# Optimization experiments

Measured on AMD Instinct MI355X. Metric: run time of the kernel, lower is better.

The kernel has to match this reference:

```python
import jax, jax.numpy as jnp
import numpy as np

D = 128          # node_state_dim
N_NODES = 5000
WINDOW = 10
N_TOTAL = WINDOW * N_NODES
E = 131072       # structural (int) edges
T = 2            # message passing steps
HID = 1024


def setup_inputs() -> dict:
    key = jax.random.key(0)
    ks = jax.random.split(key, 20)
    ie = jax.random.randint(ks[0], (E, 3), 0, N_NODES, dtype=jnp.int32)
    int_edges = jnp.stack([ie[:, 0] % WINDOW, ie[:, 1], ie[:, 2]], axis=1)
    nodes = jax.random.randint(ks[1], (N_NODES,), 0, 10, dtype=jnp.int32)

    def init(k, shape, scale=0.05):
        return (jax.random.normal(k, shape, jnp.float32) * scale)

    params = dict(
        embed_table=init(ks[2], (10, D)),
        msg_W1=init(ks[3], (2 * D, HID)), msg_b1=jnp.zeros((HID,), jnp.float32),
        msg_W2=init(ks[4], (HID, D)), msg_b2=jnp.zeros((D,), jnp.float32),
        gru_int_W=init(ks[5], (D, 3 * D)), gru_int_U=init(ks[6], (D, 3 * D)),
        gru_int_b=jnp.zeros((2, 3 * D), jnp.float32),
        gru_temp_W=init(ks[7], (D, 3 * D)), gru_temp_U=init(ks[8], (D, 3 * D)),
        gru_temp_b=jnp.zeros((2, 3 * D), jnp.float32),
        ro_W1=init(ks[9], (D, HID)), ro_b1=jnp.zeros((HID,), jnp.float32),
        ro_W2=init(ks[10], (HID, 512)), ro_b2=jnp.zeros((512,), jnp.float32),
        ro_W3=init(ks[11], (512, 10)), ro_b3=jnp.zeros((10,), jnp.float32),
    )
    return {"int_edges": int_edges, "nodes": nodes, **params}


def _temp_edges():
    fwd_src = np.arange(0, N_TOTAL - N_NODES)
    fwd_dst = fwd_src + N_NODES
    bwd_src = np.arange(N_NODES, N_TOTAL)
    bwd_dst = bwd_src - N_NODES
    src = jnp.asarray(np.concatenate([fwd_src, bwd_src]), jnp.int32)
    dst = jnp.asarray(np.concatenate([fwd_dst, bwd_dst]), jnp.int32)
    return src, dst


def _gru(x, h, W, U, b):
    # Keras GRUCell, reset_after=True. x,h: [N,D]; W,U: [D,3D]; b: [2,3D]
    xg = x @ W + b[0]
    hg = h @ U + b[1]
    xz, xr, xh = jnp.split(xg, 3, axis=-1)
    hz, hr, hh = jnp.split(hg, 3, axis=-1)
    z = jax.nn.sigmoid(xz + hz)
    r = jax.nn.sigmoid(xr + hr)
    hcand = jnp.tanh(xh + r * hh)
    return z * h + (1.0 - z) * hcand


def _msg(x, W1, b1, W2, b2):
    # Dense(1024,relu) -> Dropout(inference: identity) -> Dense(D,relu)
    return jax.nn.relu(jax.nn.relu(x @ W1 + b1) @ W2 + b2)


def _seg_mean(x, idx, n):
    s = jax.ops.segment_sum(x, idx, num_segments=n)
    c = jax.ops.segment_sum(jnp.ones((x.shape[0],), x.dtype), idx, num_segments=n)
    return jnp.where(c[:, None] > 0, s / jnp.maximum(c, 1.0)[:, None], 0.0)


def reference(int_edges, nodes, embed_table, msg_W1, msg_b1, msg_W2, msg_b2,
              gru_int_W, gru_int_U, gru_int_b, gru_temp_W, gru_temp_U, gru_temp_b,
              ro_W1, ro_b1, ro_W2, ro_b2, ro_W3, ro_b3):
    node_idx = int_edges[:, 0] * N_NODES + int_edges[:, 1]        # [E]
    neigh_idx = int_edges[:, 0] * N_NODES + int_edges[:, 2]       # [E]
    t_src, t_dst = _temp_edges()

    h = embed_table[nodes]                                        # [n_nodes, D]
    h = jnp.repeat(h, WINDOW, axis=0)                             # [N_TOTAL, D]

    for _ in range(T):
        # structural edges
        m_in = jnp.concatenate([h[node_idx], h[neigh_idx]], axis=1)   # [E, 2D]
        m = _msg(m_in, msg_W1, msg_b1, msg_W2, msg_b2)                # [E, D]
        agg = _seg_mean(m, neigh_idx, N_TOTAL)                        # [N_TOTAL, D]
        h = _gru(agg, h, gru_int_W, gru_int_U, gru_int_b)
        # temporal edges
        tm_in = jnp.concatenate([h[t_src], h[t_dst]], axis=1)
        tm = _msg(tm_in, msg_W1, msg_b1, msg_W2, msg_b2)
        tagg = _seg_mean(tm, t_dst, N_TOTAL)
        h = _gru(tagg, h, gru_temp_W, gru_temp_U, gru_temp_b)

    # readout on first frame's nodes
    x = h[:N_NODES]
    x = jax.nn.relu(x @ ro_W1 + ro_b1)
    x = jax.nn.relu(x @ ro_W2 + ro_b2)
    return jax.nn.softmax(x @ ro_W3 + ro_b3, axis=-1)
```

## Files before the change

kernel.cpp:

```cpp
#include <hip/hip_runtime.h>
#include <math.h>

#define D 128
#define N_NODES 5000
#define WINDOW 10
#define N_TOTAL 50000
#define NE_INT 131072
#define NE_TMP 90000
#define NE_FWD (N_TOTAL - N_NODES)
#define HID 1024

typedef short bf16x8 __attribute__((ext_vector_type(8)));
typedef float f32x4 __attribute__((ext_vector_type(4)));

#define SA 264
#define SH 136
#define SK 136
#define SCAN_B 256

static __device__ __forceinline__ short f2bf(float f) {
    union { float f; unsigned u; } v; v.f = f;
    unsigned r = v.u + 0x7fffu + ((v.u >> 16) & 1u);
    return (short)(r >> 16);
}
static __device__ __forceinline__ float bf2f(short s) {
    union { unsigned u; float f; } v;
    v.u = ((unsigned)(unsigned short)s) << 16;
    return v.f;
}

__global__ void k_tcvt(const float* __restrict__ in, short* __restrict__ out, int K, int N) {
    int i = blockIdx.x * blockDim.x + threadIdx.x;
    if (i >= N * K) return;
    int n = i / K, k = i - n * K;
    out[i] = f2bf(in[(size_t)k * N + n]);
}

__global__ void k_init_h(const int* __restrict__ nodes, const float* __restrict__ embed,
                         float* __restrict__ h32, short* __restrict__ h16) {
    int i = blockIdx.x * blockDim.x + threadIdx.x;
    if (i >= N_TOTAL * D) return;
    int row = i >> 7;
    int c = i & 127;
    int n = nodes[row / WINDOW];
    float v = embed[n * D + c];
    h32[i] = v;
    h16[i] = f2bf(v);
}

__global__ void k_build_int_edges(const int* __restrict__ ie, int* __restrict__ src,
                                  int* __restrict__ dst, int* __restrict__ icnt) {
    int e = blockIdx.x * blockDim.x + threadIdx.x;
    if (e >= NE_INT) return;
    int t = ie[e * 3 + 0], a = ie[e * 3 + 1], b = ie[e * 3 + 2];
    int d = t * N_NODES + b;
    src[e] = t * N_NODES + a;
    dst[e] = d;
    atomicAdd(&icnt[d], 1);
}

__global__ void k_build_tmp_edges(int* __restrict__ src, int* __restrict__ dst) {
    int e = blockIdx.x * blockDim.x + threadIdx.x;
    if (e >= NE_TMP) return;
    int s, d;
    if (e < NE_FWD) { s = e; d = e + N_NODES; }
    else { int q = e - NE_FWD; s = q + N_NODES; d = q; }
    src[e] = s;
    dst[e] = d;
}

__global__ void k_scan_partial(const int* __restrict__ cnt, int* __restrict__ rowstart,
                               int* __restrict__ btot, int n) {
    __shared__ int s[SCAN_B];
    int tid = threadIdx.x;
    int i = blockIdx.x * SCAN_B + tid;
    int v = (i < n) ? cnt[i] : 0;
    s[tid] = v;
    __syncthreads();
    for (int off = 1; off < SCAN_B; off <<= 1) {
        int x = (tid >= off) ? s[tid - off] : 0;
        __syncthreads();
        s[tid] += x;
        __syncthreads();
    }
    if (i < n) rowstart[i] = s[tid] - v;
    if (tid == SCAN_B - 1) btot[blockIdx.x] = s[tid];
}

__global__ void k_scan_block(int* __restrict__ btot, int nb) {
    __shared__ int s[SCAN_B];
    int tid = threadIdx.x;
    int v = (tid < nb) ? btot[tid] : 0;
    s[tid] = v;
    __syncthreads();
    for (int off = 1; off < SCAN_B; off <<= 1) {
        int x = (tid >= off) ? s[tid - off] : 0;
        __syncthreads();
        s[tid] += x;
        __syncthreads();
    }
    if (tid < nb) btot[tid] = s[tid] - v;
}

__global__ void k_scan_add(int* __restrict__ rowstart, const int* __restrict__ btot,
                           int* __restrict__ cursor, int n, int total) {
    int i = blockIdx.x * blockDim.x + threadIdx.x;
    if (i < n) {
        int v = rowstart[i] + btot[i >> 8];
        rowstart[i] = v;
        cursor[i] = v;
    }
    if (i == 0) rowstart[n] = total;
}

__global__ void k_fill_csr(const int* __restrict__ dst, int nE, int* __restrict__ cursor,
                           int* __restrict__ eidx) {
    int e = blockIdx.x * blockDim.x + threadIdx.x;
    if (e >= nE) return;
    int p = atomicAdd(&cursor[dst[e]], 1);
    eidx[p] = e;
}

__global__ void __launch_bounds__(256, 2) k_msg_mfma(
    const short* __restrict__ h16, const int* __restrict__ src, const int* __restrict__ dst,
    int nE, const short* __restrict__ W1T, const float* __restrict__ b1,
    const short* __restrict__ W2T, const float* __restrict__ b2,
    short* __restrict__ m)
{
    __shared__ short Ain[64 * SA];
    __shared__ short Hid[64 * SH];

    int t = threadIdx.x;
    int e0 = blockIdx.x * 64;

    {
        int r = t >> 2, q = t & 3;
        int e = e0 + r;
        int ec = (e < nE) ? e : (nE - 1);
        int s = src[ec], d = dst[ec];
        const uint4* ps = (const uint4*)(h16 + (size_t)s * D);
        const uint4* pd = (const uint4*)(h16 + (size_t)d * D);
        uint4* ao = (uint4*)(Ain + r * SA);
#pragma unroll
        for (int i = 0; i < 8; ++i) {
            int g = i * 4 + q;
            ao[g] = (i < 4) ? ps[g] : pd[g - 16];
        }
    }
    __syncthreads();

    int w = t >> 6, lane = t & 63;
    int lm = lane & 15, lk = lane >> 4;

    f32x4 c2[2][4];
#pragma unroll
    for (int cs = 0; cs < 2; ++cs) {
        int out0 = w * 32 + cs * 16 + lk * 4;
#pragma unroll
        for (int et = 0; et < 4; ++et)
#pragma unroll
            for (int rg = 0; rg < 4; ++rg) c2[cs][et][rg] = b2[out0 + rg];
    }

    for (int hc = 0; hc < 8; ++hc) {
        f32x4 c1[2][4];
#pragma unroll
        for (int cs = 0; cs < 2; ++cs) {
            int ch0 = hc * 128 + (2 * w + cs) * 16 + lk * 4;
#pragma unroll
            for (int et = 0; et < 4; ++et)
#pragma unroll
                for (int rg = 0; rg < 4; ++rg) c1[cs][et][rg] = b1[ch0 + rg];
        }
#pragma unroll
        for (int kk = 0; kk < 8; ++kk) {
            int ko = kk * 32 + lk * 8;
            bf16x8 a0 = *(const bf16x8*)(W1T + (size_t)(hc * 128 + (2 * w) * 16 + lm) * 256 + ko);
            bf16x8 a1 = *(const bf16x8*)(W1T + (size_t)(hc * 128 + (2 * w + 1) * 16 + lm) * 256 + ko);
            bf16x8 bf[4];
#pragma unroll
            for (int et = 0; et < 4; ++et)
                bf[et] = *(const bf16x8*)(Ain + (et * 16 + lm) * SA + ko);
#pragma unroll
            for (int et = 0; et < 4; ++et) {
                c1[0][et] = __builtin_amdgcn_mfma_f32_16x16x32_bf16(a0, bf[et], c1[0][et], 0, 0, 0);
                c1[1][et] = __builtin_amdgcn_mfma_f32_16x16x32_bf16(a1, bf[et], c1[1][et], 0, 0, 0);
            }
        }
        __syncthreads();
#pragma unroll
        for (int cs = 0; cs < 2; ++cs) {
            int ch_in = (2 * w + cs) * 16 + lk * 4;
#pragma unroll
            for (int et = 0; et < 4; ++et) {
                int edge = et * 16 + lm;
                short4 sv;
                sv.x = f2bf(fmaxf(c1[cs][et][0], 0.f));
                sv.y = f2bf(fmaxf(c1[cs][et][1], 0.f));
                sv.z = f2bf(fmaxf(c1[cs][et][2], 0.f));
                sv.w = f2bf(fmaxf(c1[cs][et][3], 0.f));
                *(short4*)(Hid + edge * SH + ch_in) = sv;
            }
        }
        __syncthreads();
#pragma unroll
        for (int kk = 0; kk < 4; ++kk) {
            int ko = kk * 32 + lk * 8;
            bf16x8 a0 = *(const bf16x8*)(W2T + (size_t)(w * 32 + lm) * 1024 + hc * 128 + ko);
            bf16x8 a1 = *(const bf16x8*)(W2T + (size_t)(w * 32 + 16 + lm) * 1024 + hc * 128 + ko);
            bf16x8 bf[4];
#pragma unroll
            for (int et = 0; et < 4; ++et)
                bf[et] = *(const bf16x8*)(Hid + (et * 16 + lm) * SH + ko);
#pragma unroll
            for (int et = 0; et < 4; ++et) {
                c2[0][et] = __builtin_amdgcn_mfma_f32_16x16x32_bf16(a0, bf[et], c2[0][et], 0, 0, 0);
                c2[1][et] = __builtin_amdgcn_mfma_f32_16x16x32_bf16(a1, bf[et], c2[1][et], 0, 0, 0);
            }
        }
    }

#pragma unroll
    for (int et = 0; et < 4; ++et) {
        int edge = et * 16 + lm;
        int e = e0 + edge;
        if (e >= nE) continue;
        short* rowp = m + (size_t)e * 128;
#pragma unroll
        for (int cs = 0; cs < 2; ++cs) {
            int out0 = w * 32 + cs * 16 + lk * 4;
            short4 sv;
            sv.x = f2bf(fmaxf(c2[cs][et][0], 0.f));
            sv.y = f2bf(fmaxf(c2[cs][et][1], 0.f));
            sv.z = f2bf(fmaxf(c2[cs][et][2], 0.f));
            sv.w = f2bf(fmaxf(c2[cs][et][3], 0.f));
            *(short4*)(rowp + out0) = sv;
        }
    }
}

__global__ void __launch_bounds__(256, 2) k_gru_mfma(
    const short* __restrict__ m, const int* __restrict__ rowstart,
    const int* __restrict__ eidx, int mode,
    float* __restrict__ h32, short* __restrict__ h16,
    const short* __restrict__ WT, const short* __restrict__ UT,
    const float* __restrict__ b)
{
    __shared__ short Ax[64 * SK];
    __shared__ short Hx[64 * SK];
    int t = threadIdx.x;
    int r0 = blockIdx.x * 64;

    {
        int r = t >> 2, q = t & 3;
        int row = r0 + r;
        int rc = (row < N_TOTAL) ? row : (N_TOTAL - 1);
        const uint4* hp = (const uint4*)(h16 + (size_t)rc * D);
        uint4* hxo = (uint4*)(Hx + r * SK);
#pragma unroll
        for (int i = 0; i < 4; ++i) hxo[q * 4 + i] = hp[q * 4 + i];

        float acc[32];
#pragma unroll
        for (int i = 0; i < 32; ++i) acc[i] = 0.f;
        int deg = 0;
        if (row < N_TOTAL) {
            if (mode == 0) {
                int s0 = rowstart[row], s1 = rowstart[row + 1];
                deg = s1 - s0;
                for (int p = s0; p < s1; ++p) {
                    int e = eidx[p];
                    const uint4* mp = (const uint4*)(m + (size_t)e * 128 + q * 32);
#pragma unroll
                    for (int i = 0; i < 4; ++i) {
                        uint4 v = mp[i];
                        const short* sp = (const short*)&v;
#pragma unroll
                        for (int j = 0; j < 8; ++j) acc[i * 8 + j] += bf2f(sp[j]);
                    }
                }
            } else {
                if (row >= N_NODES) {
                    const uint4* mp = (const uint4*)(m + (size_t)(row - N_NODES) * 128 + q * 32);
                    ++deg;
#pragma unroll
                    for (int i = 0; i < 4; ++i) {
                        uint4 v = mp[i];
                        const short* sp = (const short*)&v;
#pragma unroll
                        for (int j = 0; j < 8; ++j) acc[i * 8 + j] += bf2f(sp[j]);
                    }
                }
                if (row < NE_FWD) {
                    const uint4* mp = (const uint4*)(m + (size_t)(NE_FWD + row) * 128 + q * 32);
                    ++deg;
#pragma unroll
                    for (int i = 0; i < 4; ++i) {
                        uint4 v = mp[i];
                        const short* sp = (const short*)&v;
#pragma unroll
                        for (int j = 0; j < 8; ++j) acc[i * 8 + j] += bf2f(sp[j]);
                    }
                }
            }
        }
        float inv = (deg > 0) ? 1.f / (float)deg : 0.f;
        uint4* axp = (uint4*)(Ax + r * SK + q * 32);
#pragma unroll
        for (int i = 0; i < 4; ++i) {
            union { uint4 u; short s[8]; } pk;
#pragma unroll
            for (int j = 0; j < 8; ++j) pk.s[j] = f2bf(acc[i * 8 + j] * inv);
            axp[i] = pk.u;
        }
    }
    __syncthreads();

    int w = t >> 6, lane = t & 63;
    int lm = lane & 15, lk = lane >> 4;

    for (int g = 0; g < 8; ++g) {
        int ch = g * 16 + lm;
        f32x4 cxz, cxr, cxh, chz, chr_, chh;
#pragma unroll
        for (int rg = 0; rg < 4; ++rg) {
            cxz[rg] = b[ch];        chz[rg] = b[384 + ch];
            cxr[rg] = b[128 + ch];  chr_[rg] = b[384 + 128 + ch];
            cxh[rg] = b[256 + ch];  chh[rg] = b[384 + 256 + ch];
        }
#pragma unroll
        for (int kk = 0; kk < 4; ++kk) {
            int ko = kk * 32 + lk * 8;
            bf16x8 ax = *(const bf16x8*)(Ax + (w * 16 + lm) * SK + ko);
            bf16x8 hx = *(const bf16x8*)(Hx + (w * 16 + lm) * SK + ko);
            bf16x8 bz = *(const bf16x8*)(WT + (size_t)(ch) * 128 + ko);
            bf16x8 br = *(const bf16x8*)(WT + (size_t)(128 + ch) * 128 + ko);
            bf16x8 bh = *(const bf16x8*)(WT + (size_t)(256 + ch) * 128 + ko);
            bf16x8 uz = *(const bf16x8*)(UT + (size_t)(ch) * 128 + ko);
            bf16x8 ur = *(const bf16x8*)(UT + (size_t)(128 + ch) * 128 + ko);
            bf16x8 uh = *(const bf16x8*)(UT + (size_t)(256 + ch) * 128 + ko);
            cxz = __builtin_amdgcn_mfma_f32_16x16x32_bf16(ax, bz, cxz, 0, 0, 0);
            cxr = __builtin_amdgcn_mfma_f32_16x16x32_bf16(ax, br, cxr, 0, 0, 0);
            cxh = __builtin_amdgcn_mfma_f32_16x16x32_bf16(ax, bh, cxh, 0, 0, 0);
            chz = __builtin_amdgcn_mfma_f32_16x16x32_bf16(hx, uz, chz, 0, 0, 0);
            chr_ = __builtin_amdgcn_mfma_f32_16x16x32_bf16(hx, ur, chr_, 0, 0, 0);
            chh = __builtin_amdgcn_mfma_f32_16x16x32_bf16(hx, uh, chh, 0, 0, 0);
        }
#pragma unroll
        for (int rg = 0; rg < 4; ++rg) {
            int row = r0 + w * 16 + lk * 4 + rg;
            if (row >= N_TOTAL) continue;
            float z = 1.f / (1.f + expf(-(cxz[rg] + chz[rg])));
            float r_ = 1.f / (1.f + expf(-(cxr[rg] + chr_[rg])));
            float hcv = tanhf(cxh[rg] + r_ * chh[rg]);
            size_t idx = (size_t)row * D + ch;
            float hold = h32[idx];
            float hnew = z * hold + (1.f - z) * hcv;
            h32[idx] = hnew;
            h16[idx] = f2bf(hnew);
        }
    }
}

__global__ void __launch_bounds__(256, 2) k_ro_mfma(
    const short* __restrict__ A16, const short* __restrict__ BT,
    const float* __restrict__ bias, float* __restrict__ C32, short* __restrict__ C16,
    int M, int N, int K)
{
    __shared__ short As[64 * SK];
    int t = threadIdx.x;
    int mb = blockIdx.y * 64;
    int nb = blockIdx.x * 128;
    int w = t >> 6, lane = t & 63;
    int lm = lane & 15, lk = lane >> 4;

    f32x4 acc[8];
#pragma unroll
    for (int nt = 0; nt < 8; ++nt) {
        float bv = bias[nb + nt * 16 + lm];
        acc[nt][0] = bv; acc[nt][1] = bv; acc[nt][2] = bv; acc[nt][3] = bv;
    }

    for (int kc = 0; kc < K; kc += 128) {
        __syncthreads();
        {
            int r = t >> 2, q = t & 3;
            int row = mb + r;
            int rc = (row < M) ? row : (M - 1);
            const uint4* ap = (const uint4*)(A16 + (size_t)rc * K + kc);
            uint4* ao = (uint4*)(As + r * SK);
#pragma unroll
            for (int i = 0; i < 4; ++i) ao[i * 4 + q] = ap[i * 4 + q];
        }
        __syncthreads();
#pragma unroll
        for (int kk = 0; kk < 4; ++kk) {
            int ko = kk * 32 + lk * 8;
            bf16x8 a = *(const bf16x8*)(As + (w * 16 + lm) * SK + ko);
#pragma unroll
            for (int nt = 0; nt < 8; ++nt) {
                bf16x8 bfr = *(const bf16x8*)(BT + (size_t)(nb + nt * 16 + lm) * K + kc + ko);
                acc[nt] = __builtin_amdgcn_mfma_f32_16x16x32_bf16(a, bfr, acc[nt], 0, 0, 0);
            }
        }
    }
#pragma unroll
    for (int nt = 0; nt < 8; ++nt) {
        int col = nb + nt * 16 + lm;
#pragma unroll
        for (int rg = 0; rg < 4; ++rg) {
            int row = mb + w * 16 + lk * 4 + rg;
            if (row >= M) continue;
            float v = fmaxf(acc[nt][rg], 0.f);
            if (C32) C32[(size_t)row * N + col] = v;
            if (C16) C16[(size_t)row * N + col] = f2bf(v);
        }
    }
}

__global__ void __launch_bounds__(64) k_logits_softmax(
    const float* __restrict__ r2, const float* __restrict__ W3,
    const float* __restrict__ b3, float* __restrict__ out)
{
    int row = blockIdx.x;
    int t = threadIdx.x;
    float p[10];
#pragma unroll
    for (int j = 0; j < 10; ++j) p[j] = 0.f;
    for (int k = t; k < 512; k += 64) {
        float v = r2[(size_t)row * 512 + k];
#pragma unroll
        for (int j = 0; j < 10; ++j) p[j] += v * W3[k * 10 + j];
    }
#pragma unroll
    for (int j = 0; j < 10; ++j) {
        float s = p[j];
        for (int off = 32; off > 0; off >>= 1) s += __shfl_down(s, off);
        p[j] = s;
    }
    if (t == 0) {
        float mx = -1e30f;
#pragma unroll
        for (int j = 0; j < 10; ++j) { p[j] += b3[j]; mx = fmaxf(mx, p[j]); }
        float sum = 0.f;
#pragma unroll
        for (int j = 0; j < 10; ++j) { p[j] = expf(p[j] - mx); sum += p[j]; }
        float inv = 1.f / sum;
#pragma unroll
        for (int j = 0; j < 10; ++j) out[(size_t)row * 10 + j] = p[j] * inv;
    }
}

extern "C" void kernel_launch(void* const* d_in, const int* in_sizes, int n_in,
                              void* d_out, int out_size, void* d_ws, size_t ws_size,
                              hipStream_t stream)
{
    const int*   ie    = (const int*)d_in[0];
    const int*   nodes = (const int*)d_in[1];
    const float* embed = (const float*)d_in[2];
    const float* mW1   = (const float*)d_in[3];
    const float* mb1   = (const float*)d_in[4];
    const float* mW2   = (const float*)d_in[5];
    const float* mb2   = (const float*)d_in[6];
    const float* giW   = (const float*)d_in[7];
    const float* giU   = (const float*)d_in[8];
    const float* gib   = (const float*)d_in[9];
    const float* gtW   = (const float*)d_in[10];
    const float* gtU   = (const float*)d_in[11];
    const float* gtb   = (const float*)d_in[12];
    const float* rW1   = (const float*)d_in[13];
    const float* rb1   = (const float*)d_in[14];
    const float* rW2   = (const float*)d_in[15];
    const float* rb2   = (const float*)d_in[16];
    const float* rW3   = (const float*)d_in[17];
    const float* rb3   = (const float*)d_in[18];
    float* out = (float*)d_out;

    char* ws = (char*)d_ws;
    size_t off = 0;
    auto alloc = [&](size_t bytes) {
        void* p = ws + off;
        off += (bytes + 255) & ~(size_t)255;
        return p;
    };
    float* h32   = (float*)alloc((size_t)N_TOTAL * D * 4);
    short* h16   = (short*)alloc((size_t)N_TOTAL * D * 2);
    short* m     = (short*)alloc((size_t)NE_INT * 128 * 2);
    int*   icnt  = (int*)alloc((size_t)N_TOTAL * 4);
    int*   rowst = (int*)alloc((size_t)(N_TOTAL + 1) * 4);
    int*   btot  = (int*)alloc(256 * 4);
    int*   curs  = (int*)alloc((size_t)N_TOTAL * 4);
    int*   eidx  = (int*)alloc((size_t)NE_INT * 4);
    int*   srcA  = (int*)alloc((size_t)NE_INT * 4);
    int*   dstA  = (int*)alloc((size_t)NE_INT * 4);
    int*   srcT  = (int*)alloc((size_t)NE_TMP * 4);
    int*   dstT  = (int*)alloc((size_t)NE_TMP * 4);
    short* mW1T  = (short*)alloc((size_t)HID * 256 * 2);
    short* mW2T  = (short*)alloc((size_t)D * HID * 2);
    short* giWT  = (short*)alloc((size_t)384 * D * 2);
    short* giUT  = (short*)alloc((size_t)384 * D * 2);
    short* gtWT  = (short*)alloc((size_t)384 * D * 2);
    short* gtUT  = (short*)alloc((size_t)384 * D * 2);
    short* rW1T  = (short*)alloc((size_t)HID * D * 2);
    short* rW2T  = (short*)alloc((size_t)512 * HID * 2);
    short* r1_16 = (short*)alloc((size_t)N_NODES * HID * 2);
    float* r2_32 = (float*)alloc((size_t)N_NODES * 512 * 4);

    auto tc = [&](const float* in, short* o, int K, int N) {
        k_tcvt<<<(N * K + 255) / 256, 256, 0, stream>>>(in, o, K, N);
    };
    tc(mW1, mW1T, 256, HID);
    tc(mW2, mW2T, HID, D);
    tc(giW, giWT, D, 384);
    tc(giU, giUT, D, 384);
    tc(gtW, gtWT, D, 384);
    tc(gtU, gtUT, D, 384);
    tc(rW1, rW1T, D, HID);
    tc(rW2, rW2T, HID, 512);

    hipMemsetAsync(icnt, 0, (size_t)N_TOTAL * 4, stream);
    k_init_h<<<(N_TOTAL * D + 255) / 256, 256, 0, stream>>>(nodes, embed, h32, h16);
    k_build_int_edges<<<(NE_INT + 255) / 256, 256, 0, stream>>>(ie, srcA, dstA, icnt);
    k_build_tmp_edges<<<(NE_TMP + 255) / 256, 256, 0, stream>>>(srcT, dstT);
    int nb = (N_TOTAL + SCAN_B - 1) / SCAN_B;
    k_scan_partial<<<nb, SCAN_B, 0, stream>>>(icnt, rowst, btot, N_TOTAL);
    k_scan_block<<<1, SCAN_B, 0, stream>>>(btot, nb);
    k_scan_add<<<nb, SCAN_B, 0, stream>>>(rowst, btot, curs, N_TOTAL, NE_INT);
    k_fill_csr<<<(NE_INT + 255) / 256, 256, 0, stream>>>(dstA, NE_INT, curs, eidx);

    int gmsgA = (NE_INT + 63) / 64;
    int gmsgT = (NE_TMP + 63) / 64;
    int ggru = (N_TOTAL + 63) / 64;
    for (int it = 0; it < 2; ++it) {
        k_msg_mfma<<<gmsgA, 256, 0, stream>>>(h16, srcA, dstA, NE_INT, mW1T, mb1, mW2T, mb2, m);
        k_gru_mfma<<<ggru, 256, 0, stream>>>(m, rowst, eidx, 0, h32, h16, giWT, giUT, gib);

        k_msg_mfma<<<gmsgT, 256, 0, stream>>>(h16, srcT, dstT, NE_TMP, mW1T, mb1, mW2T, mb2, m);
        k_gru_mfma<<<ggru, 256, 0, stream>>>(m, rowst, eidx, 1, h32, h16, gtWT, gtUT, gtb);
    }

    dim3 g1(HID / 128, (N_NODES + 63) / 64);
    k_ro_mfma<<<g1, 256, 0, stream>>>(h16, rW1T, rb1, (float*)nullptr, r1_16, N_NODES, HID, D);
    dim3 g2(512 / 128, (N_NODES + 63) / 64);
    k_ro_mfma<<<g2, 256, 0, stream>>>(r1_16, rW2T, rb2, r2_32, (short*)nullptr, N_NODES, 512, HID);
    k_logits_softmax<<<N_NODES, 64, 0, stream>>>(r2_32, rW3, rb3, out);
}
```

Measured before the change: 1.295 ms.

## Keep gathered message inputs in registers and double-buffer swizzled hidden tile

The message MLP kernel now gathers each edge's src/dst node states straight from global memory into MFMA B-fragment registers, so the staging LDS tile and its sync are gone. The hidden-activation LDS tile is double-buffered by chunk parity, which drops one barrier per chunk. It is stored with an XOR swizzle instead of padding to avoid bank conflicts. Biases are added at the ReLU epilogue instead of being used to initialise the accumulators. This holds 32 extra bf16x8 vectors in registers per thread, which raises register pressure under launch_bounds(256,2) and risks spills or lower occupancy.

```diff
diff --git a/kernel.cpp b/kernel.cpp
--- a/kernel.cpp
+++ b/kernel.cpp
@@ -13,8 +13,6 @@
 typedef short bf16x8 __attribute__((ext_vector_type(8)));
 typedef float f32x4 __attribute__((ext_vector_type(4)));
 
-#define SA 264
-#define SH 136
 #define SK 136
 #define SCAN_B 256
 
@@ -127,79 +125,71 @@
     const short* __restrict__ W2T, const float* __restrict__ b2,
     short* __restrict__ m)
 {
-    __shared__ short Ain[64 * SA];
-    __shared__ short Hid[64 * SH];
+    __shared__ short Hid[2][64 * 128];
 
     int t = threadIdx.x;
     int e0 = blockIdx.x * 64;
-
-    {
-        int r = t >> 2, q = t & 3;
-        int e = e0 + r;
-        int ec = (e < nE) ? e : (nE - 1);
-        int s = src[ec], d = dst[ec];
-        const uint4* ps = (const uint4*)(h16 + (size_t)s * D);
-        const uint4* pd = (const uint4*)(h16 + (size_t)d * D);
-        uint4* ao = (uint4*)(Ain + r * SA);
-#pragma unroll
-        for (int i = 0; i < 8; ++i) {
-            int g = i * 4 + q;
-            ao[g] = (i < 4) ? ps[g] : pd[g - 16];
-        }
-    }
-    __syncthreads();
-
     int w = t >> 6, lane = t & 63;
     int lm = lane & 15, lk = lane >> 4;
 
+    bf16x8 bfrag[4][8];
+#pragma unroll
+    for (int et = 0; et < 4; ++et) {
+        int e = e0 + et * 16 + lm;
+        int ec = (e < nE) ? e : (nE - 1);
+        const short* ps = h16 + (size_t)src[ec] * D;
+        const short* pd = h16 + (size_t)dst[ec] * D;
+#pragma unroll
+        for (int kk = 0; kk < 4; ++kk)
+            bfrag[et][kk] = *(const bf16x8*)(ps + kk * 32 + lk * 8);
+#pragma unroll
+        for (int kk = 4; kk < 8; ++kk)
+            bfrag[et][kk] = *(const bf16x8*)(pd + (kk - 4) * 32 + lk * 8);
+    }
+
     f32x4 c2[2][4];
 #pragma unroll
-    for (int cs = 0; cs < 2; ++cs) {
-        int out0 = w * 32 + cs * 16 + lk * 4;
+    for (int cs = 0; cs < 2; ++cs)
 #pragma unroll
         for (int et = 0; et < 4; ++et)
 #pragma unroll
-            for (int rg = 0; rg < 4; ++rg) c2[cs][et][rg] = b2[out0 + rg];
-    }
+            for (int rg = 0; rg < 4; ++rg) c2[cs][et][rg] = 0.f;
 
     for (int hc = 0; hc < 8; ++hc) {
         f32x4 c1[2][4];
 #pragma unroll
-        for (int cs = 0; cs < 2; ++cs) {
-            int ch0 = hc * 128 + (2 * w + cs) * 16 + lk * 4;
+        for (int cs = 0; cs < 2; ++cs)
 #pragma unroll
             for (int et = 0; et < 4; ++et)
 #pragma unroll
-                for (int rg = 0; rg < 4; ++rg) c1[cs][et][rg] = b1[ch0 + rg];
-        }
+                for (int rg = 0; rg < 4; ++rg) c1[cs][et][rg] = 0.f;
 #pragma unroll
         for (int kk = 0; kk < 8; ++kk) {
             int ko = kk * 32 + lk * 8;
             bf16x8 a0 = *(const bf16x8*)(W1T + (size_t)(hc * 128 + (2 * w) * 16 + lm) * 256 + ko);
             bf16x8 a1 = *(const bf16x8*)(W1T + (size_t)(hc * 128 + (2 * w + 1) * 16 + lm) * 256 + ko);
-            bf16x8 bf[4];
-#pragma unroll
-            for (int et = 0; et < 4; ++et)
-                bf[et] = *(const bf16x8*)(Ain + (et * 16 + lm) * SA + ko);
 #pragma unroll
             for (int et = 0; et < 4; ++et) {
-                c1[0][et] = __builtin_amdgcn_mfma_f32_16x16x32_bf16(a0, bf[et], c1[0][et], 0, 0, 0);
-                c1[1][et] = __builtin_amdgcn_mfma_f32_16x16x32_bf16(a1, bf[et], c1[1][et], 0, 0, 0);
+                c1[0][et] = __builtin_amdgcn_mfma_f32_16x16x32_bf16(a0, bfrag[et][kk], c1[0][et], 0, 0, 0);
+                c1[1][et] = __builtin_amdgcn_mfma_f32_16x16x32_bf16(a1, bfrag[et][kk], c1[1][et], 0, 0, 0);
             }
         }
-        __syncthreads();
+        short* hbuf = (short*)Hid[hc & 1];
 #pragma unroll
         for (int cs = 0; cs < 2; ++cs) {
-            int ch_in = (2 * w + cs) * 16 + lk * 4;
+            int chl = (2 * w + cs) * 16 + lk * 4;
+            float4 bq = *(const float4*)(b1 + hc * 128 + chl);
+            int qw = chl >> 3;
+            int sub = chl & 7;
 #pragma unroll
             for (int et = 0; et < 4; ++et) {
                 int edge = et * 16 + lm;
                 short4 sv;
-                sv.x = f2bf(fmaxf(c1[cs][et][0], 0.f));
-                sv.y = f2bf(fmaxf(c1[cs][et][1], 0.f));
-                sv.z = f2bf(fmaxf(c1[cs][et][2], 0.f));
-                sv.w = f2bf(fmaxf(c1[cs][et][3], 0.f));
-                *(short4*)(Hid + edge * SH + ch_in) = sv;
+                sv.x = f2bf(fmaxf(c1[cs][et][0] + bq.x, 0.f));
+                sv.y = f2bf(fmaxf(c1[cs][et][1] + bq.y, 0.f));
+                sv.z = f2bf(fmaxf(c1[cs][et][2] + bq.z, 0.f));
+                sv.w = f2bf(fmaxf(c1[cs][et][3] + bq.w, 0.f));
+                *(short4*)(hbuf + edge * 128 + ((qw ^ (edge & 15)) << 3) + sub) = sv;
             }
         }
         __syncthreads();
@@ -208,14 +198,13 @@
             int ko = kk * 32 + lk * 8;
             bf16x8 a0 = *(const bf16x8*)(W2T + (size_t)(w * 32 + lm) * 1024 + hc * 128 + ko);
             bf16x8 a1 = *(const bf16x8*)(W2T + (size_t)(w * 32 + 16 + lm) * 1024 + hc * 128 + ko);
-            bf16x8 bf[4];
-#pragma unroll
-            for (int et = 0; et < 4; ++et)
-                bf[et] = *(const bf16x8*)(Hid + (et * 16 + lm) * SH + ko);
+            int q = kk * 4 + lk;
 #pragma unroll
             for (int et = 0; et < 4; ++et) {
-                c2[0][et] = __builtin_amdgcn_mfma_f32_16x16x32_bf16(a0, bf[et], c2[0][et], 0, 0, 0);
-                c2[1][et] = __builtin_amdgcn_mfma_f32_16x16x32_bf16(a1, bf[et], c2[1][et], 0, 0, 0);
+                int edge = et * 16 + lm;
+                bf16x8 bf = *(const bf16x8*)(hbuf + edge * 128 + ((q ^ (edge & 15)) << 3));
+                c2[0][et] = __builtin_amdgcn_mfma_f32_16x16x32_bf16(a0, bf, c2[0][et], 0, 0, 0);
+                c2[1][et] = __builtin_amdgcn_mfma_f32_16x16x32_bf16(a1, bf, c2[1][et], 0, 0, 0);
             }
         }
     }
@@ -229,11 +218,12 @@
 #pragma unroll
         for (int cs = 0; cs < 2; ++cs) {
             int out0 = w * 32 + cs * 16 + lk * 4;
+            float4 bq = *(const float4*)(b2 + out0);
             short4 sv;
-            sv.x = f2bf(fmaxf(c2[cs][et][0], 0.f));
-            sv.y = f2bf(fmaxf(c2[cs][et][1], 0.f));
-            sv.z = f2bf(fmaxf(c2[cs][et][2], 0.f));
-            sv.w = f2bf(fmaxf(c2[cs][et][3], 0.f));
+            sv.x = f2bf(fmaxf(c2[cs][et][0] + bq.x, 0.f));
+            sv.y = f2bf(fmaxf(c2[cs][et][1] + bq.y, 0.f));
+            sv.z = f2bf(fmaxf(c2[cs][et][2] + bq.z, 0.f));
+            sv.w = f2bf(fmaxf(c2[cs][et][3] + bq.w, 0.f));
             *(short4*)(rowp + out0) = sv;
         }
     }
```

Result: slower. 1.415 ms (+9.2%).
